# Kernel tuning notes

Hardware: AMD Instinct MI355X
Metric: run time of the kernel (lower is better)

The kernel has to match this reference:

```python
import jax, jax.numpy as jnp
import numpy as np

N_ATOM = 10000
N_EDGE = 40000
D = 64          # fingerprint_dim
BOND_DIM = 10
EPS_BN = 1e-6
EPS_SM = 1e-8


def _bn(x, g, b, m, v):
    # BatchNorm1d in eval mode with running stats
    return (x - m) * jax.lax.rsqrt(v + EPS_BN) * g + b


def setup_inputs() -> dict:
    key = jax.random.key(0)
    ks = jax.random.split(key, 16)
    s = 0.05
    inp = {
        "atom": jax.random.normal(ks[0], (N_ATOM, D), jnp.float32),
        "bond_index": jax.random.randint(ks[1], (N_EDGE, 2), 0, N_ATOM, jnp.int64),
        "bond": jax.random.normal(ks[2], (N_EDGE, BOND_DIM), jnp.float32),
        # encoder: Linear(bond_dim, D*D) + BN(D*D)
        "enc_W": jax.random.normal(ks[3], (D * D, BOND_DIM), jnp.float32) * s,
        "enc_b": jnp.zeros((D * D,), jnp.float32),
        "bn1_g": jnp.ones((D * D,), jnp.float32),
        "bn1_b": jnp.zeros((D * D,), jnp.float32),
        "bn1_m": jnp.zeros((D * D,), jnp.float32),
        "bn1_v": jnp.ones((D * D,), jnp.float32),
        # align: Linear(2D, 1)
        "align_W": jax.random.normal(ks[4], (1, 2 * D), jnp.float32) * s,
        "align_b": jnp.zeros((1,), jnp.float32),
        # attend: Linear(D, D) + BN(D)
        "att_W": jax.random.normal(ks[5], (D, D), jnp.float32) * s,
        "att_b": jnp.zeros((D,), jnp.float32),
        "bn2_g": jnp.ones((D,), jnp.float32),
        "bn2_b": jnp.zeros((D,), jnp.float32),
        "bn2_m": jnp.zeros((D,), jnp.float32),
        "bn2_v": jnp.ones((D,), jnp.float32),
        # GRUCell(D, D)
        "gru_Wih": jax.random.normal(ks[6], (3 * D, D), jnp.float32) * s,
        "gru_Whh": jax.random.normal(ks[7], (3 * D, D), jnp.float32) * s,
        "gru_bih": jnp.zeros((3 * D,), jnp.float32),
        "gru_bhh": jnp.zeros((3 * D,), jnp.float32),
    }
    return inp


def reference(atom, bond_index, bond, enc_W, enc_b, bn1_g, bn1_b, bn1_m, bn1_v,
              align_W, align_b, att_W, att_b, bn2_g, bn2_b, bn2_m, bn2_v,
              gru_Wih, gru_Whh, gru_bih, gru_bhh):
    num_atom, atom_dim = atom.shape
    tgt = bond_index[:, 0]  # segment index (bond_index.t()[0])
    nbr = bond_index[:, 1]

    # encoder: Linear + BN + ReLU, then view as per-edge [D, D] matrices
    enc = jax.nn.relu(_bn(bond @ enc_W.T + enc_b, bn1_g, bn1_b, bn1_m, bn1_v))
    enc = enc.reshape(-1, atom_dim, atom_dim)            # [E, D, D]

    neighbor = jnp.einsum('ed,edf->ef', atom[nbr], enc)  # per-edge bmm [E, D]
    target_atom = atom[tgt]

    feat = jnp.concatenate([target_atom, neighbor], axis=-1)       # [E, 2D]
    align_score = jax.nn.leaky_relu(feat @ align_W.T + align_b)    # [E, 1]

    atend = _bn(neighbor @ att_W.T + att_b, bn2_g, bn2_b, bn2_m, bn2_v)  # [E, D]

    # segment softmax over edges grouped by target atom
    seg_max = jax.ops.segment_max(align_score, tgt, num_segments=num_atom)
    ex = jnp.exp(align_score - seg_max[tgt])
    denom = jax.ops.segment_sum(ex, tgt, num_segments=num_atom)[tgt] + EPS_SM
    w = ex / denom                                                   # [E, 1]

    context = jax.ops.segment_sum(w * atend, tgt, num_segments=num_atom)  # [N, D]
    context = jax.nn.elu(context)

    # GRUCell(context, atom)
    gi = context @ gru_Wih.T + gru_bih
    gh = atom @ gru_Whh.T + gru_bhh
    i_r, i_z, i_n = jnp.split(gi, 3, axis=-1)
    h_r, h_z, h_n = jnp.split(gh, 3, axis=-1)
    r = jax.nn.sigmoid(i_r + h_r)
    z = jax.nn.sigmoid(i_z + h_z)
    n = jnp.tanh(i_n + r * h_n)
    update = (1.0 - z) * n + z * atom
    return update
```

## Files before the change

kernel.cpp:

```cpp
#include <hip/hip_runtime.h>

#define N_ATOM 10000
#define N_EDGE 40000
#define DD 64
#define BOND_DIM 10
#define EPS_BN 1e-6f
#define EPS_SM 1e-8f
#define GA 8

typedef __attribute__((ext_vector_type(8))) short short8;
typedef __attribute__((ext_vector_type(4))) float float4v;
typedef unsigned int u32;

constexpr size_t OFF_WFRAG   = 0;
constexpr size_t OFF_ATTFRAG = 65536;
constexpr size_t OFF_ATTB    = 67584;
constexpr size_t OFF_WIHT    = 67648;
constexpr size_t OFF_WHHT    = 79936;
constexpr size_t OFF_DENOM   = 92224;
constexpr size_t OFF_CTX     = 102224;

__device__ __forceinline__ unsigned short f2bf(float x) {
    u32 u = __float_as_uint(x);
    u32 r = u + 0x7FFFu + ((u >> 16) & 1u);
    return (unsigned short)(r >> 16);
}

__global__ void fold_kernel(const float* enc_W, const float* enc_b,
                            const float* g1, const float* b1,
                            const float* m1, const float* v1,
                            const float* att_W, const float* att_b,
                            const float* g2, const float* b2v,
                            const float* m2, const float* v2,
                            const float* Wih, const float* Whh,
                            float* ws) {
    u32* wsu = (u32*)ws;
    size_t i = (size_t)blockIdx.x * 256 + threadIdx.x;
    if (i < 16384) {
        int ch = i >> 6, l = i & 63, q = l >> 4;
        int c = (ch << 4) + (l & 15);
        float s = g1[c] * rsqrtf(v1[c] + EPS_BN);
        float bias = enc_b[c] * s + b1[c] - m1[c] * s;
        unsigned short h[8];
#pragma unroll
        for (int j = 0; j < 8; j++) {
            int k = 8 * q + j;
            float v = (k < BOND_DIM) ? enc_W[c * BOND_DIM + k] * s
                                     : ((k == BOND_DIM) ? bias : 0.f);
            h[j] = f2bf(v);
        }
#pragma unroll
        for (int m = 0; m < 4; m++)
            wsu[OFF_WFRAG + i * 4 + m] = (u32)h[2 * m] | ((u32)h[2 * m + 1] << 16);
    } else if (i < 16896) {
        int idx = i - 16384;
        int l = idx & 63, fckh = idx >> 6;
        int fc = fckh >> 1, kh = fckh & 1, q = l >> 4;
        int n = (fc << 4) + (l & 15);
        float s = g2[n] * rsqrtf(v2[n] + EPS_BN);
        unsigned short h[8];
#pragma unroll
        for (int j = 0; j < 8; j++) {
            int k = 32 * kh + 8 * q + j;
            h[j] = f2bf(att_W[n * DD + k] * s);
        }
#pragma unroll
        for (int m = 0; m < 4; m++)
            wsu[OFF_ATTFRAG + (size_t)idx * 4 + m] = (u32)h[2 * m] | ((u32)h[2 * m + 1] << 16);
    } else if (i < 16960) {
        int f = i - 16896;
        float s = g2[f] * rsqrtf(v2[f] + EPS_BN);
        ws[OFF_ATTB + f] = att_b[f] * s + b2v[f] - m2[f] * s;
    } else if (i < 29248) {
        int j = i - 16960;
        int d = j / 192, t = j % 192;
        ws[OFF_WIHT + j] = Wih[t * DD + d];
    } else if (i < 41536) {
        int j = i - 29248;
        int d = j / 192, t = j % 192;
        ws[OFF_WHHT + j] = Whh[t * DD + d];
    } else {
        size_t z = i - 41536;
        if (z < (size_t)N_ATOM + (size_t)N_ATOM * DD) ws[OFF_DENOM + z] = 0.f;
    }
}

__global__ __launch_bounds__(256) void edge_kernel(
    const float* atom, const int* bidx, const float* bond,
    const float* alignW, const float* alignb,
    const float* ws, float* denom, float* ctx) {
    __shared__ float s_bond[32][BOND_DIM];
    __shared__ float s_anbr[32][65];
    __shared__ float s_nbp[2][32][65];
    __shared__ float s_ex[32];
    __shared__ int   s_tgt[32];

    const int t = threadIdx.x;
    const int lane = t & 63;
    const int wave = t >> 6;
    const int g = wave >> 1;
    const int h = wave & 1;
    const int q = lane >> 4;
    const int r16 = lane & 15;
    const int g16 = g * 16;
    const int e0 = blockIdx.x * 32;

    for (int idx = t; idx < 32 * BOND_DIM; idx += 256)
        s_bond[idx / BOND_DIM][idx % BOND_DIM] = bond[(size_t)e0 * BOND_DIM + idx];
    if (t < 32) s_tgt[t] = bidx[2 * (e0 + t)];
    for (int e = wave; e < 32; e += 4) {
        int nbr = bidx[2 * (e0 + e) + 1];
        s_anbr[e][lane] = atom[(size_t)nbr * DD + lane];
    }
    __syncthreads();

    short8 afrag;
#pragma unroll
    for (int j = 0; j < 8; j++) {
        int k = 8 * q + j;
        unsigned short hh = 0;
        if (k < BOND_DIM) hh = f2bf(s_bond[g16 + r16][k]);
        else if (k == BOND_DIM) hh = 0x3F80u;
        afrag[j] = (short)hh;
    }

    const short8* wfrag = (const short8*)((const u32*)ws + OFF_WFRAG);
    const float4v zero4 = {0.f, 0.f, 0.f, 0.f};
    float4v nacc[4] = {zero4, zero4, zero4, zero4};
    const int d0 = 32 * h;

    auto compute = [&](const short8 cur[4], int d) {
        float av0 = s_anbr[g16 + 4 * q + 0][d];
        float av1 = s_anbr[g16 + 4 * q + 1][d];
        float av2 = s_anbr[g16 + 4 * q + 2][d];
        float av3 = s_anbr[g16 + 4 * q + 3][d];
#pragma unroll
        for (int fc = 0; fc < 4; fc++) {
            float4v e4 = __builtin_amdgcn_mfma_f32_16x16x32_bf16(afrag, cur[fc], zero4, 0, 0, 0);
            nacc[fc][0] = fmaf(av0, fmaxf(e4[0], 0.f), nacc[fc][0]);
            nacc[fc][1] = fmaf(av1, fmaxf(e4[1], 0.f), nacc[fc][1]);
            nacc[fc][2] = fmaf(av2, fmaxf(e4[2], 0.f), nacc[fc][2]);
            nacc[fc][3] = fmaf(av3, fmaxf(e4[3], 0.f), nacc[fc][3]);
        }
    };

    short8 cur[4], nxt[4];
#pragma unroll
    for (int fc = 0; fc < 4; fc++) cur[fc] = wfrag[(size_t)(d0 * 4 + fc) * 64 + lane];
#pragma unroll 2
    for (int it = 0; it < 31; it++) {
        int d = d0 + it;
#pragma unroll
        for (int fc = 0; fc < 4; fc++) nxt[fc] = wfrag[(size_t)((d + 1) * 4 + fc) * 64 + lane];
        compute(cur, d);
#pragma unroll
        for (int fc = 0; fc < 4; fc++) cur[fc] = nxt[fc];
    }
    compute(cur, d0 + 31);

#pragma unroll
    for (int fc = 0; fc < 4; fc++)
#pragma unroll
        for (int r = 0; r < 4; r++)
            s_nbp[h][g16 + 4 * q + r][fc * 16 + r16] = nacc[fc][r];
    __syncthreads();

    float4v att[4];
    if (h == 0) {
        short8 na[2];
#pragma unroll
        for (int kh = 0; kh < 2; kh++)
#pragma unroll
            for (int j = 0; j < 8; j++) {
                int k = 32 * kh + 8 * q + j;
                na[kh][j] = (short)f2bf(s_nbp[0][g16 + r16][k] + s_nbp[1][g16 + r16][k]);
            }
        const short8* battfrag = (const short8*)((const u32*)ws + OFF_ATTFRAG);
#pragma unroll
        for (int fc = 0; fc < 4; fc++) {
            att[fc] = __builtin_amdgcn_mfma_f32_16x16x32_bf16(na[0], battfrag[(fc * 2 + 0) * 64 + lane], zero4, 0, 0, 0);
            att[fc] = __builtin_amdgcn_mfma_f32_16x16x32_bf16(na[1], battfrag[(fc * 2 + 1) * 64 + lane], att[fc], 0, 0, 0);
            float ab = ws[OFF_ATTB + fc * 16 + r16];
#pragma unroll
            for (int r = 0; r < 4; r++) att[fc][r] += ab;
        }
    } else {
        const float aw1 = alignW[lane];
        const float aw2 = alignW[64 + lane];
        const float alb = alignb[0];
#pragma unroll 4
        for (int e = 0; e < 16; e++) {
            int le = g16 + e;
            int tgt = s_tgt[le];
            float nbv = s_nbp[0][le][lane] + s_nbp[1][le][lane];
            float v = atom[(size_t)tgt * DD + lane] * aw1 + nbv * aw2;
#pragma unroll
            for (int off = 32; off > 0; off >>= 1) v += __shfl_xor(v, off);
            float sc = v + alb;
            sc = sc > 0.f ? sc : 0.01f * sc;
            float ex = expf(sc);
            if (lane == 0) {
                s_ex[le] = ex;
                atomicAdd(&denom[tgt], ex);
            }
        }
    }
    __syncthreads();

    if (h == 0) {
#pragma unroll
        for (int r = 0; r < 4; r++) {
            float exr = s_ex[g16 + 4 * q + r];
            int tg = s_tgt[g16 + 4 * q + r];
#pragma unroll
            for (int fc = 0; fc < 4; fc++)
                atomicAdd(&ctx[(size_t)tg * DD + fc * 16 + r16], exr * att[fc][r]);
        }
    }
}

__global__ __launch_bounds__(192) void gru_kernel(
    const float* atom, const float* ws, const float* denom, const float* ctx,
    const float* bih, const float* bhh, float* out) {
    __shared__ float sctx[GA][DD];
    __shared__ float satom[GA][DD];
    __shared__ float sgi[GA][192];
    __shared__ float sgh[GA][192];
    const int a0 = blockIdx.x * GA;
    const int t = threadIdx.x;

    for (int idx = t; idx < GA * DD; idx += 192) {
        int a = idx >> 6, f = idx & 63;
        float c = ctx[(size_t)(a0 + a) * DD + f] / (denom[a0 + a] + EPS_SM);
        sctx[a][f] = c > 0.f ? c : expm1f(c);
        satom[a][f] = atom[(size_t)(a0 + a) * DD + f];
    }
    __syncthreads();

    const float* wiht = ws + OFF_WIHT;
    const float* whht = ws + OFF_WHHT;
    float gi[GA], gh[GA];
    const float bi = bih[t], bh = bhh[t];
#pragma unroll
    for (int a = 0; a < GA; a++) { gi[a] = bi; gh[a] = bh; }
#pragma unroll 4
    for (int d = 0; d < DD; d++) {
        float wi = wiht[d * 192 + t];
        float wh = whht[d * 192 + t];
#pragma unroll
        for (int a = 0; a < GA; a++) {
            gi[a] = fmaf(wi, sctx[a][d], gi[a]);
            gh[a] = fmaf(wh, satom[a][d], gh[a]);
        }
    }
#pragma unroll
    for (int a = 0; a < GA; a++) { sgi[a][t] = gi[a]; sgh[a][t] = gh[a]; }
    __syncthreads();

    for (int idx = t; idx < GA * DD; idx += 192) {
        int a = idx >> 6, f = idx & 63;
        float r = 1.f / (1.f + expf(-(sgi[a][f] + sgh[a][f])));
        float z = 1.f / (1.f + expf(-(sgi[a][64 + f] + sgh[a][64 + f])));
        float n = tanhf(sgi[a][128 + f] + r * sgh[a][128 + f]);
        out[(size_t)(a0 + a) * DD + f] = (1.f - z) * n + z * satom[a][f];
    }
}

extern "C" void kernel_launch(void* const* d_in, const int* in_sizes, int n_in,
                              void* d_out, int out_size, void* d_ws, size_t ws_size,
                              hipStream_t stream) {
    const float* atom   = (const float*)d_in[0];
    const int*   bidx   = (const int*)d_in[1];
    const float* bond   = (const float*)d_in[2];
    const float* enc_W  = (const float*)d_in[3];
    const float* enc_b  = (const float*)d_in[4];
    const float* bn1_g  = (const float*)d_in[5];
    const float* bn1_b  = (const float*)d_in[6];
    const float* bn1_m  = (const float*)d_in[7];
    const float* bn1_v  = (const float*)d_in[8];
    const float* alignW = (const float*)d_in[9];
    const float* alignb = (const float*)d_in[10];
    const float* att_W  = (const float*)d_in[11];
    const float* att_b  = (const float*)d_in[12];
    const float* bn2_g  = (const float*)d_in[13];
    const float* bn2_b  = (const float*)d_in[14];
    const float* bn2_m  = (const float*)d_in[15];
    const float* bn2_v  = (const float*)d_in[16];
    const float* gWih   = (const float*)d_in[17];
    const float* gWhh   = (const float*)d_in[18];
    const float* gbih   = (const float*)d_in[19];
    const float* gbhh   = (const float*)d_in[20];

    float* ws  = (float*)d_ws;
    float* out = (float*)d_out;

    fold_kernel<<<2702, 256, 0, stream>>>(enc_W, enc_b, bn1_g, bn1_b, bn1_m, bn1_v,
                                          att_W, att_b, bn2_g, bn2_b, bn2_m, bn2_v,
                                          gWih, gWhh, ws);

    edge_kernel<<<N_EDGE / 32, 256, 0, stream>>>(
        atom, bidx, bond, alignW, alignb, ws,
        ws + OFF_DENOM, ws + OFF_CTX);

    gru_kernel<<<N_ATOM / GA, 192, 0, stream>>>(atom, ws, ws + OFF_DENOM, ws + OFF_CTX,
                                                gbih, gbhh, out);
}
```

Measured before the change: 163.3 us.

## Switch edge encoder MFMA to 32x32x16 with two-wave blocks

The per-edge encoder now runs as 32x32x16 bf16 MFMAs. Each block uses 2 waves instead of 4, and each wave covers all 32 edges for half of the d range. The folded encoder weights are stored as 32x32 A-fragments with only the K=16 padding, which halves the weight workspace read per d. The attention projection and align-score phases are now split across both waves by edge half instead of by role. The intent is fewer MFMA issues and less weight-fragment traffic per edge. The cost is fewer waves per block and larger accumulator register use (32 floats per lane).

```diff
diff --git a/kernel.cpp b/kernel.cpp
--- a/kernel.cpp
+++ b/kernel.cpp
@@ -10,15 +10,16 @@
 
 typedef __attribute__((ext_vector_type(8))) short short8;
 typedef __attribute__((ext_vector_type(4))) float float4v;
+typedef __attribute__((ext_vector_type(16))) float float16v;
 typedef unsigned int u32;
 
-constexpr size_t OFF_WFRAG   = 0;
-constexpr size_t OFF_ATTFRAG = 65536;
-constexpr size_t OFF_ATTB    = 67584;
-constexpr size_t OFF_WIHT    = 67648;
-constexpr size_t OFF_WHHT    = 79936;
-constexpr size_t OFF_DENOM   = 92224;
-constexpr size_t OFF_CTX     = 102224;
+constexpr size_t OFF_AFRAG   = 0;
+constexpr size_t OFF_ATTFRAG = 32768;
+constexpr size_t OFF_ATTB    = 34816;
+constexpr size_t OFF_WIHT    = 34880;
+constexpr size_t OFF_WHHT    = 47168;
+constexpr size_t OFF_DENOM   = 59456;
+constexpr size_t OFF_CTX     = 69456;
 
 __device__ __forceinline__ unsigned short f2bf(float x) {
     u32 u = __float_as_uint(x);
@@ -36,24 +37,26 @@
                             float* ws) {
     u32* wsu = (u32*)ws;
     size_t i = (size_t)blockIdx.x * 256 + threadIdx.x;
-    if (i < 16384) {
-        int ch = i >> 6, l = i & 63, q = l >> 4;
-        int c = (ch << 4) + (l & 15);
+    if (i < 8192) {
+        int d = i >> 7, rem = i & 127;
+        int ch = rem >> 6, l = rem & 63;
+        int c = d * 64 + ch * 32 + (l & 31);
+        int kb = 8 * (l >> 5);
         float s = g1[c] * rsqrtf(v1[c] + EPS_BN);
         float bias = enc_b[c] * s + b1[c] - m1[c] * s;
         unsigned short h[8];
 #pragma unroll
         for (int j = 0; j < 8; j++) {
-            int k = 8 * q + j;
+            int k = kb + j;
             float v = (k < BOND_DIM) ? enc_W[c * BOND_DIM + k] * s
                                      : ((k == BOND_DIM) ? bias : 0.f);
             h[j] = f2bf(v);
         }
 #pragma unroll
         for (int m = 0; m < 4; m++)
-            wsu[OFF_WFRAG + i * 4 + m] = (u32)h[2 * m] | ((u32)h[2 * m + 1] << 16);
-    } else if (i < 16896) {
-        int idx = i - 16384;
+            wsu[OFF_AFRAG + i * 4 + m] = (u32)h[2 * m] | ((u32)h[2 * m + 1] << 16);
+    } else if (i < 8704) {
+        int idx = i - 8192;
         int l = idx & 63, fckh = idx >> 6;
         int fc = fckh >> 1, kh = fckh & 1, q = l >> 4;
         int n = (fc << 4) + (l & 15);
@@ -67,25 +70,25 @@
 #pragma unroll
         for (int m = 0; m < 4; m++)
             wsu[OFF_ATTFRAG + (size_t)idx * 4 + m] = (u32)h[2 * m] | ((u32)h[2 * m + 1] << 16);
-    } else if (i < 16960) {
-        int f = i - 16896;
+    } else if (i < 8768) {
+        int f = i - 8704;
         float s = g2[f] * rsqrtf(v2[f] + EPS_BN);
         ws[OFF_ATTB + f] = att_b[f] * s + b2v[f] - m2[f] * s;
-    } else if (i < 29248) {
-        int j = i - 16960;
+    } else if (i < 21056) {
+        int j = i - 8768;
         int d = j / 192, t = j % 192;
         ws[OFF_WIHT + j] = Wih[t * DD + d];
-    } else if (i < 41536) {
-        int j = i - 29248;
+    } else if (i < 33344) {
+        int j = i - 21056;
         int d = j / 192, t = j % 192;
         ws[OFF_WHHT + j] = Whh[t * DD + d];
     } else {
-        size_t z = i - 41536;
+        size_t z = i - 33344;
         if (z < (size_t)N_ATOM + (size_t)N_ATOM * DD) ws[OFF_DENOM + z] = 0.f;
     }
 }
 
-__global__ __launch_bounds__(256) void edge_kernel(
+__global__ __launch_bounds__(128) void edge_kernel(
     const float* atom, const int* bidx, const float* bond,
     const float* alignW, const float* alignb,
     const float* ws, float* denom, float* ctx) {
@@ -97,125 +100,117 @@
 
     const int t = threadIdx.x;
     const int lane = t & 63;
-    const int wave = t >> 6;
-    const int g = wave >> 1;
-    const int h = wave & 1;
+    const int h = t >> 6;
+    const int e0 = blockIdx.x * 32;
+
+    for (int idx = t; idx < 32 * BOND_DIM; idx += 128)
+        s_bond[idx / BOND_DIM][idx % BOND_DIM] = bond[(size_t)e0 * BOND_DIM + idx];
+    if (t < 32) s_tgt[t] = bidx[2 * (e0 + t)];
+    for (int e = h; e < 32; e += 2) {
+        int nbr = bidx[2 * (e0 + e) + 1];
+        s_anbr[e][lane] = atom[(size_t)nbr * DD + lane];
+    }
+    __syncthreads();
+
+    const int eb = lane & 31;
+    const int kb = 8 * (lane >> 5);
+    short8 bfrag;
+#pragma unroll
+    for (int j = 0; j < 8; j++) {
+        int k = kb + j;
+        unsigned short hh = 0;
+        if (k < BOND_DIM) hh = f2bf(s_bond[eb][k]);
+        else if (k == BOND_DIM) hh = 0x3F80u;
+        bfrag[j] = (short)hh;
+    }
+
+    const short8* afrag = (const short8*)((const u32*)ws + OFF_AFRAG);
+    float16v zero16 = {};
+    float nb0[16] = {}, nb1[16] = {};
+    const int d0 = 32 * h;
+
+    short8 a0 = afrag[(size_t)(d0 * 2 + 0) * 64 + lane];
+    short8 a1 = afrag[(size_t)(d0 * 2 + 1) * 64 + lane];
+#pragma unroll 2
+    for (int it = 0; it < 32; it++) {
+        int d = d0 + it;
+        short8 n0, n1;
+        if (it < 31) {
+            n0 = afrag[(size_t)((d + 1) * 2 + 0) * 64 + lane];
+            n1 = afrag[(size_t)((d + 1) * 2 + 1) * 64 + lane];
+        }
+        float av = s_anbr[eb][d];
+        float16v enc0 = __builtin_amdgcn_mfma_f32_32x32x16_bf16(a0, bfrag, zero16, 0, 0, 0);
+        float16v enc1 = __builtin_amdgcn_mfma_f32_32x32x16_bf16(a1, bfrag, zero16, 0, 0, 0);
+#pragma unroll
+        for (int r = 0; r < 16; r++) {
+            nb0[r] = fmaf(av, fmaxf(enc0[r], 0.f), nb0[r]);
+            nb1[r] = fmaf(av, fmaxf(enc1[r], 0.f), nb1[r]);
+        }
+        a0 = n0; a1 = n1;
+    }
+
+    const int fro = 4 * (lane >> 5);
+#pragma unroll
+    for (int r = 0; r < 16; r++) {
+        int f = (r & 3) + 8 * (r >> 2) + fro;
+        s_nbp[h][eb][f] = nb0[r];
+        s_nbp[h][eb][32 + f] = nb1[r];
+    }
+    __syncthreads();
+
+    const int es = h * 16;
     const int q = lane >> 4;
     const int r16 = lane & 15;
-    const int g16 = g * 16;
-    const int e0 = blockIdx.x * 32;
-
-    for (int idx = t; idx < 32 * BOND_DIM; idx += 256)
-        s_bond[idx / BOND_DIM][idx % BOND_DIM] = bond[(size_t)e0 * BOND_DIM + idx];
-    if (t < 32) s_tgt[t] = bidx[2 * (e0 + t)];
-    for (int e = wave; e < 32; e += 4) {
-        int nbr = bidx[2 * (e0 + e) + 1];
-        s_anbr[e][lane] = atom[(size_t)nbr * DD + lane];
-    }
-    __syncthreads();
-
-    short8 afrag;
-#pragma unroll
-    for (int j = 0; j < 8; j++) {
-        int k = 8 * q + j;
-        unsigned short hh = 0;
-        if (k < BOND_DIM) hh = f2bf(s_bond[g16 + r16][k]);
-        else if (k == BOND_DIM) hh = 0x3F80u;
-        afrag[j] = (short)hh;
-    }
-
-    const short8* wfrag = (const short8*)((const u32*)ws + OFF_WFRAG);
+
+    short8 na[2];
+#pragma unroll
+    for (int kh = 0; kh < 2; kh++)
+#pragma unroll
+        for (int j = 0; j < 8; j++) {
+            int k = 32 * kh + 8 * q + j;
+            na[kh][j] = (short)f2bf(s_nbp[0][es + r16][k] + s_nbp[1][es + r16][k]);
+        }
+    const short8* battfrag = (const short8*)((const u32*)ws + OFF_ATTFRAG);
     const float4v zero4 = {0.f, 0.f, 0.f, 0.f};
-    float4v nacc[4] = {zero4, zero4, zero4, zero4};
-    const int d0 = 32 * h;
-
-    auto compute = [&](const short8 cur[4], int d) {
-        float av0 = s_anbr[g16 + 4 * q + 0][d];
-        float av1 = s_anbr[g16 + 4 * q + 1][d];
-        float av2 = s_anbr[g16 + 4 * q + 2][d];
-        float av3 = s_anbr[g16 + 4 * q + 3][d];
-#pragma unroll
-        for (int fc = 0; fc < 4; fc++) {
-            float4v e4 = __builtin_amdgcn_mfma_f32_16x16x32_bf16(afrag, cur[fc], zero4, 0, 0, 0);
-            nacc[fc][0] = fmaf(av0, fmaxf(e4[0], 0.f), nacc[fc][0]);
-            nacc[fc][1] = fmaf(av1, fmaxf(e4[1], 0.f), nacc[fc][1]);
-            nacc[fc][2] = fmaf(av2, fmaxf(e4[2], 0.f), nacc[fc][2]);
-            nacc[fc][3] = fmaf(av3, fmaxf(e4[3], 0.f), nacc[fc][3]);
-        }
-    };
-
-    short8 cur[4], nxt[4];
-#pragma unroll
-    for (int fc = 0; fc < 4; fc++) cur[fc] = wfrag[(size_t)(d0 * 4 + fc) * 64 + lane];
-#pragma unroll 2
-    for (int it = 0; it < 31; it++) {
-        int d = d0 + it;
-#pragma unroll
-        for (int fc = 0; fc < 4; fc++) nxt[fc] = wfrag[(size_t)((d + 1) * 4 + fc) * 64 + lane];
-        compute(cur, d);
-#pragma unroll
-        for (int fc = 0; fc < 4; fc++) cur[fc] = nxt[fc];
-    }
-    compute(cur, d0 + 31);
-
-#pragma unroll
-    for (int fc = 0; fc < 4; fc++)
-#pragma unroll
-        for (int r = 0; r < 4; r++)
-            s_nbp[h][g16 + 4 * q + r][fc * 16 + r16] = nacc[fc][r];
-    __syncthreads();
-
     float4v att[4];
-    if (h == 0) {
-        short8 na[2];
-#pragma unroll
-        for (int kh = 0; kh < 2; kh++)
-#pragma unroll
-            for (int j = 0; j < 8; j++) {
-                int k = 32 * kh + 8 * q + j;
-                na[kh][j] = (short)f2bf(s_nbp[0][g16 + r16][k] + s_nbp[1][g16 + r16][k]);
-            }
-        const short8* battfrag = (const short8*)((const u32*)ws + OFF_ATTFRAG);
-#pragma unroll
-        for (int fc = 0; fc < 4; fc++) {
-            att[fc] = __builtin_amdgcn_mfma_f32_16x16x32_bf16(na[0], battfrag[(fc * 2 + 0) * 64 + lane], zero4, 0, 0, 0);
-            att[fc] = __builtin_amdgcn_mfma_f32_16x16x32_bf16(na[1], battfrag[(fc * 2 + 1) * 64 + lane], att[fc], 0, 0, 0);
-            float ab = ws[OFF_ATTB + fc * 16 + r16];
-#pragma unroll
-            for (int r = 0; r < 4; r++) att[fc][r] += ab;
-        }
-    } else {
-        const float aw1 = alignW[lane];
-        const float aw2 = alignW[64 + lane];
-        const float alb = alignb[0];
+#pragma unroll
+    for (int fc = 0; fc < 4; fc++) {
+        att[fc] = __builtin_amdgcn_mfma_f32_16x16x32_bf16(na[0], battfrag[(fc * 2 + 0) * 64 + lane], zero4, 0, 0, 0);
+        att[fc] = __builtin_amdgcn_mfma_f32_16x16x32_bf16(na[1], battfrag[(fc * 2 + 1) * 64 + lane], att[fc], 0, 0, 0);
+        float ab = ws[OFF_ATTB + fc * 16 + r16];
+#pragma unroll
+        for (int r = 0; r < 4; r++) att[fc][r] += ab;
+    }
+
+    const float aw1 = alignW[lane];
+    const float aw2 = alignW[64 + lane];
+    const float alb = alignb[0];
 #pragma unroll 4
-        for (int e = 0; e < 16; e++) {
-            int le = g16 + e;
-            int tgt = s_tgt[le];
-            float nbv = s_nbp[0][le][lane] + s_nbp[1][le][lane];
-            float v = atom[(size_t)tgt * DD + lane] * aw1 + nbv * aw2;
-#pragma unroll
-            for (int off = 32; off > 0; off >>= 1) v += __shfl_xor(v, off);
-            float sc = v + alb;
-            sc = sc > 0.f ? sc : 0.01f * sc;
-            float ex = expf(sc);
-            if (lane == 0) {
-                s_ex[le] = ex;
-                atomicAdd(&denom[tgt], ex);
-            }
-        }
-    }
-    __syncthreads();
-
-    if (h == 0) {
-#pragma unroll
-        for (int r = 0; r < 4; r++) {
-            float exr = s_ex[g16 + 4 * q + r];
-            int tg = s_tgt[g16 + 4 * q + r];
-#pragma unroll
-            for (int fc = 0; fc < 4; fc++)
-                atomicAdd(&ctx[(size_t)tg * DD + fc * 16 + r16], exr * att[fc][r]);
-        }
+    for (int e = 0; e < 16; e++) {
+        int le = es + e;
+        int tgt = s_tgt[le];
+        float nbv = s_nbp[0][le][lane] + s_nbp[1][le][lane];
+        float v = atom[(size_t)tgt * DD + lane] * aw1 + nbv * aw2;
+#pragma unroll
+        for (int off = 32; off > 0; off >>= 1) v += __shfl_xor(v, off);
+        float sc = v + alb;
+        sc = sc > 0.f ? sc : 0.01f * sc;
+        float ex = expf(sc);
+        if (lane == 0) {
+            s_ex[le] = ex;
+            atomicAdd(&denom[tgt], ex);
+        }
+    }
+
+#pragma unroll
+    for (int r = 0; r < 4; r++) {
+        int le = es + 4 * q + r;
+        float exr = s_ex[le];
+        int tg = s_tgt[le];
+#pragma unroll
+        for (int fc = 0; fc < 4; fc++)
+            atomicAdd(&ctx[(size_t)tg * DD + fc * 16 + r16], exr * att[fc][r]);
     }
 }
 
@@ -294,11 +289,11 @@
     float* ws  = (float*)d_ws;
     float* out = (float*)d_out;
 
-    fold_kernel<<<2702, 256, 0, stream>>>(enc_W, enc_b, bn1_g, bn1_b, bn1_m, bn1_v,
+    fold_kernel<<<2670, 256, 0, stream>>>(enc_W, enc_b, bn1_g, bn1_b, bn1_m, bn1_v,
                                           att_W, att_b, bn2_g, bn2_b, bn2_m, bn2_v,
                                           gWih, gWhh, ws);
 
-    edge_kernel<<<N_EDGE / 32, 256, 0, stream>>>(
+    edge_kernel<<<N_EDGE / 32, 128, 0, stream>>>(
         atom, bidx, bond, alignW, alignb, ws,
         ws + OFF_DENOM, ws + OFF_CTX);
 
```

New measurement: 164.5 us. About the same (+0.8%).
